# Optimization experiments

Hardware: AMD Instinct MI355X
Metric: run time of the kernel (lower is better)

## Reference

```python
import jax, jax.numpy as jnp
import numpy as np

N = 16384        # num particles (nodes)
E = 65536        # num edges (avg degree 4)
C = 32           # channels
IC = 64          # inter_channels
K = 16           # kernel taps = 4*4
EPS = 1e-5       # haiku BatchNorm default eps


def _conv_params(key, c_in, c_out):
    k1, k2 = jax.random.split(key)
    W = jax.random.normal(k1, (K, c_in, c_out), jnp.float32) / np.sqrt(K * c_in)
    P = jax.random.normal(k2, (3, K), jnp.float32)   # rel_pos -> kernel tap logits
    b = jnp.zeros((c_out,), jnp.float32)
    return W, P, b


def _bn_params(key, dim):
    k1, k2 = jax.random.split(key)
    scale = jnp.ones((dim,), jnp.float32)
    offset = jnp.zeros((dim,), jnp.float32)
    mean = 0.1 * jax.random.normal(k1, (dim,), jnp.float32)
    var = jax.random.uniform(k2, (dim,), jnp.float32, 0.5, 1.5)
    return scale, offset, mean, var


def setup_inputs() -> dict:
    key = jax.random.key(0)
    ks = jax.random.split(key, 16)
    d = {}
    d['x'] = jax.random.normal(ks[0], (N, C), jnp.float32)
    d['y'] = jax.random.normal(ks[1], (N, C), jnp.float32)
    d['senders'] = jax.random.randint(ks[2], (E,), 0, N)
    d['receivers'] = jax.random.randint(ks[3], (E,), 0, N)
    d['rel_pos'] = jax.random.normal(ks[4], (E, 3), jnp.float32)
    d['a'] = jax.random.uniform(ks[5], (E,), jnp.float32)
    dims = [(2 * C, IC), (IC, C), (C, IC), (IC, C)]
    for i, (ci, co) in enumerate(dims, start=1):
        W, P, b = _conv_params(ks[5 + i], ci, co)
        d[f'W{i}'], d[f'P{i}'], d[f'b{i}'] = W, P, b
        s, o, m, v = _bn_params(ks[9 + i], co)
        d[f's{i}'], d[f'o{i}'], d[f'm{i}'], d[f'v{i}'] = s, o, m, v
    return d


def _cconv(feat, senders, receivers, rel_pos, a, W, P, b):
    # Continuous conv: gather sender features, interpolate K kernel taps
    # from rel_pos, per-edge contraction, weight by a, scatter-add to receivers.
    fe = feat[senders]                                  # (E, Cin) gather
    w = jax.nn.softmax(rel_pos @ P, axis=-1)            # (E, K) tap weights
    fw = fe[:, None, :] * w[:, :, None]                 # (E, K, Cin)
    oe = jnp.einsum('eki,kio->eo', fw, W) * a[:, None]  # (E, Cout)
    return jax.ops.segment_sum(oe, receivers, num_segments=N) + b


def _bn(h, scale, offset, mean, var):
    # haiku BatchNorm, is_training=False (moving-average stats)
    return (h - mean) * jax.lax.rsqrt(var + EPS) * scale + offset


def reference(x, y, rel_pos, a,
              W1, P1, b1, s1, o1, m1, v1,
              W2, P2, b2, s2, o2, m2, v2,
              W3, P3, b3, s3, o3, m3, v3,
              W4, P4, b4, s4, o4, m4, v4,
              senders, receivers):
    xa = jnp.concatenate([x, y], axis=-1)               # (N, 2C)
    xl = _cconv(xa, senders, receivers, rel_pos, a, W1, P1, b1)
    xl = jax.nn.relu(_bn(xl, s1, o1, m1, v1))
    xl = _cconv(xl, senders, receivers, rel_pos, a, W2, P2, b2)
    xl = _bn(xl, s2, o2, m2, v2)
    wei1 = jax.nn.sigmoid(xl)
    xo = 2.0 * x * wei1 + 2.0 * y * (1.0 - wei1)        # first AFF fusion
    xl2 = _cconv(xo, senders, receivers, rel_pos, a, W3, P3, b3)
    xl2 = jax.nn.relu(_bn(xl2, s3, o3, m3, v3))
    xl2 = _cconv(xl2, senders, receivers, rel_pos, a, W4, P4, b4)
    xl2 = _bn(xl2, s4, o4, m4, v4)
    wei2 = jax.nn.sigmoid(xl2)
    return 2.0 * x * wei2 + 2.0 * y * (1.0 - wei2)      # second AFF fusion
```

## Files before the change

### kernel.cpp

```cpp
#include <hip/hip_runtime.h>
#include <hip/hip_bf16.h>

#define NN 16384
#define NE 65536

typedef __attribute__((ext_vector_type(8))) short short8;
typedef __attribute__((ext_vector_type(4))) float f32x4;

using bf16 = __hip_bfloat16;

__device__ __forceinline__ float b2f(bf16 v){ return __bfloat162float(v); }
__device__ __forceinline__ bf16 f2b(float v){ return __float2bfloat16(v); }

__global__ __launch_bounds__(256) void k_setup(
    const int* __restrict__ recv, const int* __restrict__ send,
    unsigned* __restrict__ curs, unsigned* __restrict__ csr,
    const float* __restrict__ rel, const float* __restrict__ a,
    const float* __restrict__ P1, const float* __restrict__ P2,
    const float* __restrict__ P3, const float* __restrict__ P4,
    float* __restrict__ g,
    const float* __restrict__ W1, const float* __restrict__ W2,
    const float* __restrict__ W3, const float* __restrict__ W4,
    bf16* __restrict__ Bp,
    const float* __restrict__ x, const float* __restrict__ y,
    bf16* __restrict__ xyc)
{
    int b = blockIdx.x;
    if(b < 256){
        int e = b*256 + threadIdx.x;
        int rv = recv[e];
        unsigned pos = atomicAdd(&curs[rv], 1u);
        if(pos < 32u) csr[(unsigned)rv*32u + pos] = ((unsigned)e << 14) | (unsigned)send[e];
        float r0 = rel[e*3+0], r1 = rel[e*3+1], r2 = rel[e*3+2];
        float av = a[e];
        const float* Ps[4] = {P1,P2,P3,P4};
        for(int c=0;c<4;c++){
            const float* P = Ps[c];
            float lg[16]; float mx = -1e30f;
            #pragma unroll
            for(int k=0;k<16;k++){
                float v = r0*P[k] + r1*P[16+k] + r2*P[32+k];
                lg[k] = v; mx = fmaxf(mx, v);
            }
            float ssum = 0.f;
            #pragma unroll
            for(int k=0;k<16;k++){ lg[k] = __expf(lg[k]-mx); ssum += lg[k]; }
            float inv = av/ssum;
            float* go = &g[((size_t)c*NE + e)*16];
            #pragma unroll
            for(int j=0;j<4;j++){
                ((float4*)go)[j] = make_float4(lg[j*4]*inv, lg[j*4+1]*inv,
                                               lg[j*4+2]*inv, lg[j*4+3]*inv);
            }
        }
        return;
    }
    if(b < 336){
        int t = (b-256)*256 + threadIdx.x;
        const float* W; int Cout; int base; int tl;
        if(t < 8192)      { W=W1; Cout=64; base=0;     tl=t; }
        else if(t < 12288){ W=W2; Cout=32; base=8192;  tl=t-8192; }
        else if(t < 16384){ W=W3; Cout=64; base=12288; tl=t-12288; }
        else              { W=W4; Cout=32; base=16384; tl=t-16384; }
        int l  = tl & 63;
        int NCT = Cout >> 4;
        int ct = (tl >> 6) % NCT;
        int ks = (tl >> 6) / NCT;
        int col = ct*16 + (l & 15);
        int k0  = ks*32 + ((l >> 4) & 3)*8;
        short8 v;
        #pragma unroll
        for(int j=0;j<8;j++){
            bf16 h = f2b(W[(size_t)(k0+j)*Cout + col]);
            v[j] = (short)*(unsigned short*)&h;
        }
        ((short8*)Bp)[base + tl] = v;
        return;
    }
    int t = (b-336)*256 + threadIdx.x;
    int n = t >> 1, half = t & 1;
    const float* src = half ? (y + n*32) : (x + n*32);
    bf16* dst = xyc + (size_t)n*64 + half*32;
    #pragma unroll
    for(int j=0;j<4;j++){
        float4 v0 = ((const float4*)src)[2*j];
        float4 v1 = ((const float4*)src)[2*j+1];
        short8 o;
        bf16 h;
        h = f2b(v0.x); o[0]=(short)*(unsigned short*)&h;
        h = f2b(v0.y); o[1]=(short)*(unsigned short*)&h;
        h = f2b(v0.z); o[2]=(short)*(unsigned short*)&h;
        h = f2b(v0.w); o[3]=(short)*(unsigned short*)&h;
        h = f2b(v1.x); o[4]=(short)*(unsigned short*)&h;
        h = f2b(v1.y); o[5]=(short)*(unsigned short*)&h;
        h = f2b(v1.z); o[6]=(short)*(unsigned short*)&h;
        h = f2b(v1.w); o[7]=(short)*(unsigned short*)&h;
        ((short8*)dst)[j] = o;
    }
}

template<int CIN, int NCT, int MODE, typename OT>
__global__ __launch_bounds__(1024, 8) void k_conv(
    const bf16* __restrict__ fAb,
    const float* __restrict__ g,
    const unsigned* __restrict__ csr, const unsigned* __restrict__ curs,
    const bf16* __restrict__ Bp, const float* __restrict__ bias,
    const float* __restrict__ bns, const float* __restrict__ bno,
    const float* __restrict__ bnm, const float* __restrict__ bnv,
    const float* __restrict__ x, const float* __restrict__ y,
    OT* __restrict__ out)
{
    constexpr int KD   = CIN*16;
    constexpr int ROWB = KD*2;
    __shared__ __align__(16) char sT[16*ROWB];
    int wv = threadIdx.x >> 6, lane = threadIdx.x & 63;
    int nbase = blockIdx.x*16;
    int node  = nbase + wv;

    const unsigned* crow = csr + (unsigned)node*32u;
    unsigned cnt = curs[node]; if(cnt > 32u) cnt = 32u;
    uint4 c0 = ((const uint4*)crow)[0];
    uint4 c1 = ((const uint4*)crow)[1];
    uint4 c2 = ((const uint4*)crow)[2];
    unsigned uu[12] = {c0.x,c0.y,c0.z,c0.w, c1.x,c1.y,c1.z,c1.w, c2.x,c2.y,c2.z,c2.w};

    const int i     = (CIN==64) ? lane : (lane & 31);
    const int kbase = (CIN==64) ? 0 : ((lane >> 5) * 8);
    constexpr int KPL = (CIN==64) ? 16 : 8;
    float acc[KPL];
    #pragma unroll
    for(int r=0;r<KPL;r++) acc[r] = 0.f;

    auto edge = [&](unsigned u){
        int sid = (int)(u & 16383u);
        int eid = (int)(u >> 14);
        float fe = b2f(fAb[sid*CIN + i]);
        const float4* gp = (const float4*)&g[(size_t)eid*16 + kbase];
        if(CIN==64){
            float4 g0=gp[0], g1=gp[1], g2=gp[2], g3=gp[3];
            acc[0]  += g0.x*fe; acc[1]  += g0.y*fe; acc[2]  += g0.z*fe; acc[3]  += g0.w*fe;
            acc[4]  += g1.x*fe; acc[5]  += g1.y*fe; acc[6]  += g1.z*fe; acc[7]  += g1.w*fe;
            acc[8]  += g2.x*fe; acc[9]  += g2.y*fe; acc[10] += g2.z*fe; acc[11] += g2.w*fe;
            acc[12] += g3.x*fe; acc[13] += g3.y*fe; acc[14] += g3.z*fe; acc[15] += g3.w*fe;
        } else {
            float4 g0=gp[0], g1=gp[1];
            acc[0] += g0.x*fe; acc[1] += g0.y*fe; acc[2] += g0.z*fe; acc[3] += g0.w*fe;
            acc[4] += g1.x*fe; acc[5] += g1.y*fe; acc[6] += g1.z*fe; acc[7] += g1.w*fe;
        }
    };
    #pragma unroll
    for(int j=0;j<12;j++){
        if((unsigned)j < cnt) edge(uu[j]);
    }
    for(unsigned j=12; j<cnt; j++) edge(crow[j]);

    unsigned xo_ = (unsigned)((wv & 7) << 4);
    if(CIN==64){
        #pragma unroll
        for(int k=0;k<16;k++){
            unsigned byte = (unsigned)wv*ROWB + ((((unsigned)(k*64 + lane))*2u) ^ xo_);
            *(bf16*)(sT + byte) = f2b(acc[k]);
        }
    } else {
        #pragma unroll
        for(int r=0;r<8;r++){
            unsigned byte = (unsigned)wv*ROWB + ((((unsigned)((kbase+r)*32 + i))*2u) ^ xo_);
            *(bf16*)(sT + byte) = f2b(acc[r]);
        }
    }
    __syncthreads();

    if(wv >= NCT) return;
    int r = lane & 15, h = lane >> 4;
    int c = wv;
    const short8* Bp8 = (const short8*)Bp;
    f32x4 acc4 = (f32x4){0.f,0.f,0.f,0.f};
    unsigned xr = (unsigned)((r & 7) << 4);
    #pragma unroll 8
    for(int ks=0; ks<KD/32; ks++){
        unsigned ab = (unsigned)r*ROWB + (((unsigned)(ks*64 + h*16)) ^ xr);
        short8 af  = *(const short8*)(sT + ab);
        short8 bfr = Bp8[(ks*NCT + c)*64 + lane];
        acc4 = __builtin_amdgcn_mfma_f32_16x16x32_bf16(af, bfr, acc4, 0, 0, 0);
    }

    const int Cout = NCT*16;
    int col = c*16 + r;
    float inv = rsqrtf(bnv[col] + 1e-5f);
    float al  = bns[col] * inv;
    float be  = al*(bias[col] - bnm[col]) + bno[col];
    #pragma unroll
    for(int j=0;j<4;j++){
        int rr = nbase + h*4 + j;
        float v = al*acc4[j] + be;
        if(MODE==0){
            out[(size_t)rr*Cout + col] = (OT)fmaxf(v, 0.f);
        } else {
            float wei = 1.f/(1.f + __expf(-v));
            float xv = x[rr*32 + col];
            float yv = y[rr*32 + col];
            out[(size_t)rr*32 + col] = (OT)(2.f*xv*wei + 2.f*yv*(1.f - wei));
        }
    }
}

extern "C" void kernel_launch(void* const* d_in, const int* in_sizes, int n_in,
                              void* d_out, int out_size, void* d_ws, size_t ws_size,
                              hipStream_t stream){
    const float* x   = (const float*)d_in[0];
    const float* y   = (const float*)d_in[1];
    const int* send  = (const int*)d_in[2];
    const int* recv  = (const int*)d_in[3];
    const float* rel = (const float*)d_in[4];
    const float* a   = (const float*)d_in[5];
    const float *W[4], *P[4], *bb[4], *bs[4], *bo[4], *bm[4], *bv[4];
    for(int i=0;i<4;i++){
        int base = 6 + i*7;
        W[i]  = (const float*)d_in[base+0];
        P[i]  = (const float*)d_in[base+1];
        bb[i] = (const float*)d_in[base+2];
        bs[i] = (const float*)d_in[base+3];
        bo[i] = (const float*)d_in[base+4];
        bm[i] = (const float*)d_in[base+5];
        bv[i] = (const float*)d_in[base+6];
    }
    char* w = (char*)d_ws;
    float*    g    = (float*)(w);
    unsigned* curs = (unsigned*)(w + 16777216);
    unsigned* csr  = (unsigned*)(w + 16842752);
    bf16*     h1   = (bf16*)(w + 18939904);
    bf16*     xo   = (bf16*)(w + 21037056);
    bf16*     h3   = (bf16*)(w + 22085632);
    bf16*     Bp   = (bf16*)(w + 24182784);
    bf16*     xyc  = (bf16*)(w + 24510464);
    float*    outp = (float*)d_out;

    hipMemsetAsync(curs, 0, NN*sizeof(unsigned), stream);
    k_setup<<<464, 256, 0, stream>>>(recv, send, curs, csr, rel, a,
                                     P[0], P[1], P[2], P[3], g,
                                     W[0], W[1], W[2], W[3], Bp,
                                     x, y, xyc);

    (k_conv<64,4,0,bf16>) <<<NN/16, 1024, 0, stream>>>(xyc, g + (size_t)0*NE*16, csr, curs,
        Bp + (size_t)0*8,     bb[0], bs[0], bo[0], bm[0], bv[0], nullptr, nullptr, h1);
    (k_conv<64,2,1,bf16>) <<<NN/16, 1024, 0, stream>>>(h1, g + (size_t)1*NE*16, csr, curs,
        Bp + (size_t)8192*8,  bb[1], bs[1], bo[1], bm[1], bv[1], x, y, xo);
    (k_conv<32,4,0,bf16>) <<<NN/16, 1024, 0, stream>>>(xo, g + (size_t)2*NE*16, csr, curs,
        Bp + (size_t)12288*8, bb[2], bs[2], bo[2], bm[2], bv[2], nullptr, nullptr, h3);
    (k_conv<64,2,1,float>)<<<NN/16, 1024, 0, stream>>>(h3, g + (size_t)3*NE*16, csr, curs,
        Bp + (size_t)16384*8, bb[3], bs[3], bo[3], bm[3], bv[3], x, y, outp);
}
```

Measured before the change: 99.70 us.

## Build CSR with LDS-local counters per node range and drop memset

CSR construction now assigns each of 32 blocks a 512-node range. Every block scans all 65536 edges and counts its own receivers with LDS atomics, so the global atomics and the separate memset launch go away. The softmax tap-weight computation is split into one thread per (edge, conv) pair to get more parallelism, and setup blocks grow to 1024 threads. The conv kernel preloads 8 CSR entries instead of 12 and relaxes the launch-bounds occupancy hint, which may reduce register pressure. The cost is that each CSR block reads the full receiver array, 32x redundant reads in total.

```diff
diff --git a/kernel.cpp b/kernel.cpp
--- a/kernel.cpp
+++ b/kernel.cpp
@@ -12,7 +12,7 @@
 __device__ __forceinline__ float b2f(bf16 v){ return __bfloat162float(v); }
 __device__ __forceinline__ bf16 f2b(float v){ return __float2bfloat16(v); }
 
-__global__ __launch_bounds__(256) void k_setup(
+__global__ __launch_bounds__(1024) void k_setup(
     const int* __restrict__ recv, const int* __restrict__ send,
     unsigned* __restrict__ curs, unsigned* __restrict__ csr,
     const float* __restrict__ rel, const float* __restrict__ a,
@@ -25,38 +25,54 @@
     const float* __restrict__ x, const float* __restrict__ y,
     bf16* __restrict__ xyc)
 {
-    int b = blockIdx.x;
-    if(b < 256){
-        int e = b*256 + threadIdx.x;
-        int rv = recv[e];
-        unsigned pos = atomicAdd(&curs[rv], 1u);
-        if(pos < 32u) csr[(unsigned)rv*32u + pos] = ((unsigned)e << 14) | (unsigned)send[e];
+    __shared__ unsigned lcnt[512];
+    int b = blockIdx.x, tid = threadIdx.x;
+
+    if(b < 32){
+        int nb = b*512;
+        if(tid < 512) lcnt[tid] = 0u;
+        __syncthreads();
+        #pragma unroll 4
+        for(int j=0; j<64; j++){
+            int e  = j*1024 + tid;
+            int rv = recv[e];
+            int lr = rv - nb;
+            if((unsigned)lr < 512u){
+                unsigned pos = atomicAdd(&lcnt[lr], 1u);
+                if(pos < 32u)
+                    csr[(unsigned)rv*32u + pos] = ((unsigned)e << 14) | (unsigned)send[e];
+            }
+        }
+        __syncthreads();
+        if(tid < 512) curs[nb + tid] = lcnt[tid];
+        return;
+    }
+    if(b < 288){
+        int task = (b-32)*1024 + tid;
+        int e = task & (NE-1), c = task >> 16;
         float r0 = rel[e*3+0], r1 = rel[e*3+1], r2 = rel[e*3+2];
         float av = a[e];
-        const float* Ps[4] = {P1,P2,P3,P4};
-        for(int c=0;c<4;c++){
-            const float* P = Ps[c];
-            float lg[16]; float mx = -1e30f;
-            #pragma unroll
-            for(int k=0;k<16;k++){
-                float v = r0*P[k] + r1*P[16+k] + r2*P[32+k];
-                lg[k] = v; mx = fmaxf(mx, v);
-            }
-            float ssum = 0.f;
-            #pragma unroll
-            for(int k=0;k<16;k++){ lg[k] = __expf(lg[k]-mx); ssum += lg[k]; }
-            float inv = av/ssum;
-            float* go = &g[((size_t)c*NE + e)*16];
-            #pragma unroll
-            for(int j=0;j<4;j++){
-                ((float4*)go)[j] = make_float4(lg[j*4]*inv, lg[j*4+1]*inv,
-                                               lg[j*4+2]*inv, lg[j*4+3]*inv);
-            }
+        const float* P = (c==0)?P1:(c==1)?P2:(c==2)?P3:P4;
+        float lg[16]; float mx = -1e30f;
+        #pragma unroll
+        for(int k=0;k<16;k++){
+            float v = r0*P[k] + r1*P[16+k] + r2*P[32+k];
+            lg[k] = v; mx = fmaxf(mx, v);
+        }
+        float ssum = 0.f;
+        #pragma unroll
+        for(int k=0;k<16;k++){ lg[k] = __expf(lg[k]-mx); ssum += lg[k]; }
+        float inv = av/ssum;
+        float* go = &g[((size_t)c*NE + e)*16];
+        #pragma unroll
+        for(int j=0;j<4;j++){
+            ((float4*)go)[j] = make_float4(lg[j*4]*inv, lg[j*4+1]*inv,
+                                           lg[j*4+2]*inv, lg[j*4+3]*inv);
         }
         return;
     }
-    if(b < 336){
-        int t = (b-256)*256 + threadIdx.x;
+    if(b < 308){
+        int t = (b-288)*1024 + tid;
         const float* W; int Cout; int base; int tl;
         if(t < 8192)      { W=W1; Cout=64; base=0;     tl=t; }
         else if(t < 12288){ W=W2; Cout=32; base=8192;  tl=t-8192; }
@@ -77,7 +93,7 @@
         ((short8*)Bp)[base + tl] = v;
         return;
     }
-    int t = (b-336)*256 + threadIdx.x;
+    int t = (b-308)*1024 + tid;
     int n = t >> 1, half = t & 1;
     const float* src = half ? (y + n*32) : (x + n*32);
     bf16* dst = xyc + (size_t)n*64 + half*32;
@@ -85,8 +101,7 @@
     for(int j=0;j<4;j++){
         float4 v0 = ((const float4*)src)[2*j];
         float4 v1 = ((const float4*)src)[2*j+1];
-        short8 o;
-        bf16 h;
+        short8 o; bf16 h;
         h = f2b(v0.x); o[0]=(short)*(unsigned short*)&h;
         h = f2b(v0.y); o[1]=(short)*(unsigned short*)&h;
         h = f2b(v0.z); o[2]=(short)*(unsigned short*)&h;
@@ -100,7 +115,7 @@
 }
 
 template<int CIN, int NCT, int MODE, typename OT>
-__global__ __launch_bounds__(1024, 8) void k_conv(
+__global__ __launch_bounds__(1024, 4) void k_conv(
     const bf16* __restrict__ fAb,
     const float* __restrict__ g,
     const unsigned* __restrict__ csr, const unsigned* __restrict__ curs,
@@ -117,15 +132,14 @@
     int nbase = blockIdx.x*16;
     int node  = nbase + wv;
 
-    const unsigned* crow = csr + (unsigned)node*32u;
-    unsigned cnt = curs[node]; if(cnt > 32u) cnt = 32u;
-    uint4 c0 = ((const uint4*)crow)[0];
-    uint4 c1 = ((const uint4*)crow)[1];
-    uint4 c2 = ((const uint4*)crow)[2];
-    unsigned uu[12] = {c0.x,c0.y,c0.z,c0.w, c1.x,c1.y,c1.z,c1.w, c2.x,c2.y,c2.z,c2.w};
-
     const int i     = (CIN==64) ? lane : (lane & 31);
     const int kbase = (CIN==64) ? 0 : ((lane >> 5) * 8);
+    unsigned cnt = curs[node]; if(cnt > 32u) cnt = 32u;
+    const unsigned* crow = csr + (unsigned)node*32u;
+    uint4 ca = ((const uint4*)crow)[0];
+    uint4 cb = ((const uint4*)crow)[1];
+    unsigned uu[8] = {ca.x, ca.y, ca.z, ca.w, cb.x, cb.y, cb.z, cb.w};
+
     constexpr int KPL = (CIN==64) ? 16 : 8;
     float acc[KPL];
     #pragma unroll
@@ -149,10 +163,10 @@
         }
     };
     #pragma unroll
-    for(int j=0;j<12;j++){
+    for(int j=0;j<8;j++){
         if((unsigned)j < cnt) edge(uu[j]);
     }
-    for(unsigned j=12; j<cnt; j++) edge(crow[j]);
+    for(unsigned j=8; j<cnt; j++) edge(crow[j]);
 
     unsigned xo_ = (unsigned)((wv & 7) << 4);
     if(CIN==64){
@@ -235,11 +249,10 @@
     bf16*     xyc  = (bf16*)(w + 24510464);
     float*    outp = (float*)d_out;
 
-    hipMemsetAsync(curs, 0, NN*sizeof(unsigned), stream);
-    k_setup<<<464, 256, 0, stream>>>(recv, send, curs, csr, rel, a,
-                                     P[0], P[1], P[2], P[3], g,
-                                     W[0], W[1], W[2], W[3], Bp,
-                                     x, y, xyc);
+    k_setup<<<340, 1024, 0, stream>>>(recv, send, curs, csr, rel, a,
+                                      P[0], P[1], P[2], P[3], g,
+                                      W[0], W[1], W[2], W[3], Bp,
+                                      x, y, xyc);
 
     (k_conv<64,4,0,bf16>) <<<NN/16, 1024, 0, stream>>>(xyc, g + (size_t)0*NE*16, csr, curs,
         Bp + (size_t)0*8,     bb[0], bs[0], bo[0], bm[0], bv[0], nullptr, nullptr, h1);
```

Measured after the change: 121.0 us. 1.21x slower.
